# Kernel optimization log

Hardware: AMD Instinct MI355X
Metric: run time of the kernel (lower is better)

## Reference

```python
import jax, jax.numpy as jnp
import numpy as np

N_NODES = 200000
N_GRAPHS = 64
IRREPS = [(64, 1), (32, 3), (16, 5)]  # (mul, 2l+1); l==0 iff dim==1
EPS = 1e-05


def setup_inputs() -> dict:
    key = jax.random.key(0)
    k1, k2, k3, k4 = jax.random.split(key, 4)
    dim_total = sum(m * d for m, d in IRREPS)  # 240
    x = jax.random.normal(k1, (N_NODES, dim_total), dtype=jnp.float32)
    batch = jnp.sort(jax.random.randint(k2, (N_NODES,), 0, N_GRAPHS))
    weight = jax.random.uniform(k3, (sum(m for m, _ in IRREPS),), dtype=jnp.float32)  # [112]
    bias = jax.random.normal(k4, (sum(m for m, d in IRREPS if d == 1),), dtype=jnp.float32)  # [64]
    return {"x": x, "batch": batch, "weight": weight, "bias": bias}


def _segment_mean(v, batch, counts):
    s = jax.ops.segment_sum(v, batch, num_segments=N_GRAPHS)
    return s / counts.reshape((-1,) + (1,) * (v.ndim - 1))


def reference(x, batch, weight, bias):
    counts = jnp.maximum(
        jax.ops.segment_sum(jnp.ones_like(batch, dtype=x.dtype), batch, num_segments=N_GRAPHS), 1.0
    )  # [B]
    out = []
    ix = iw = ib = 0
    for mul, dim in IRREPS:
        field = x[:, ix : ix + mul * dim].reshape(-1, mul, dim)  # [N, mul, dim]
        # subtract_mean=True: per-graph mean over nodes, then over multiplicity
        mean = _segment_mean(field, batch, counts).mean(axis=1, keepdims=True)  # [B,1,dim]
        field = field - mean[batch]
        if dim == 1:  # divide_norm=False, but l==0 scalars always normalized
            norm = _segment_mean(field * field, batch, counts).mean(axis=(1, 2), keepdims=True)  # [B,1,1]
            field = field / (jnp.sqrt(norm)[batch] + EPS)
        field = field * weight[iw : iw + mul][None, :, None]
        if dim == 1:
            field = field + bias[ib : ib + mul][None, :, None]
            ib += mul
        out.append(field.reshape(-1, mul * dim))
        ix += mul * dim
        iw += mul
    return jnp.concatenate(out, axis=-1)
```

## Files before the change

### kernel.cpp

```cpp
#include <hip/hip_runtime.h>

#define NGRAPH 64
#define DIMT   240
#define DIMT4  60
#define EPS    1e-5f
#define ROWS   100

typedef float f32x4 __attribute__((ext_vector_type(4)));

__global__ __launch_bounds__(256) void stats_kernel(const float* __restrict__ x,
                                                    const int* __restrict__ batch,
                                                    float* __restrict__ gstats, int n)
{
    __shared__ int    sbatch[ROWS];
    __shared__ float4 ssum[240];
    __shared__ float4 ssq[64];
    __shared__ float  lstat[12];

    const int tid = threadIdx.x;
    const int r0 = blockIdx.x * ROWS;
    const int r1 = min(n, r0 + ROWS);
    if (r0 >= n) return;
    for (int i = tid; i < r1 - r0; i += 256) sbatch[i] = batch[r0 + i];
    __syncthreads();

    const bool active = tid < 240;
    const int  r_off  = tid / 60;
    const int  j      = tid - r_off * 60;
    const float4* x4  = (const float4*)x;

    int r = r0;
    while (r < r1) {
        const int b_cur = sbatch[r - r0];
        int lo = r + 1, hi = r1;
        while (lo < hi) {
            int mid = (lo + hi) >> 1;
            if (sbatch[mid - r0] <= b_cur) lo = mid + 1; else hi = mid;
        }
        const int r_end = lo;

        float4 sum = {0.f, 0.f, 0.f, 0.f};
        float4 sq  = {0.f, 0.f, 0.f, 0.f};
        if (active) {
            const bool dosq = (j < 16);
            int rbase = r;
            for (; rbase + 16 <= r_end; rbase += 16) {
                size_t i0 = (size_t)rbase * DIMT4 + tid;
                float4 v0 = x4[i0];
                float4 v1 = x4[i0 + 240];
                float4 v2 = x4[i0 + 480];
                float4 v3 = x4[i0 + 720];
                sum.x += (v0.x + v1.x) + (v2.x + v3.x);
                sum.y += (v0.y + v1.y) + (v2.y + v3.y);
                sum.z += (v0.z + v1.z) + (v2.z + v3.z);
                sum.w += (v0.w + v1.w) + (v2.w + v3.w);
                if (dosq) {
                    sq.x = fmaf(v0.x, v0.x, fmaf(v1.x, v1.x, fmaf(v2.x, v2.x, fmaf(v3.x, v3.x, sq.x))));
                    sq.y = fmaf(v0.y, v0.y, fmaf(v1.y, v1.y, fmaf(v2.y, v2.y, fmaf(v3.y, v3.y, sq.y))));
                    sq.z = fmaf(v0.z, v0.z, fmaf(v1.z, v1.z, fmaf(v2.z, v2.z, fmaf(v3.z, v3.z, sq.z))));
                    sq.w = fmaf(v0.w, v0.w, fmaf(v1.w, v1.w, fmaf(v2.w, v2.w, fmaf(v3.w, v3.w, sq.w))));
                }
            }
            for (; rbase < r_end; rbase += 4) {
                int rr = rbase + r_off;
                if (rr < r_end) {
                    float4 v = x4[(size_t)rr * DIMT4 + j];
                    sum.x += v.x; sum.y += v.y; sum.z += v.z; sum.w += v.w;
                    if (dosq) {
                        sq.x = fmaf(v.x, v.x, sq.x); sq.y = fmaf(v.y, v.y, sq.y);
                        sq.z = fmaf(v.z, v.z, sq.z); sq.w = fmaf(v.w, v.w, sq.w);
                    }
                }
            }
        }
        if (active) ssum[tid] = sum;
        if (active && j < 16) ssq[r_off * 16 + j] = sq;
        if (tid < 12) lstat[tid] = 0.f;
        __syncthreads();
        if (tid < 60) {
            float4 t0 = ssum[tid], t1 = ssum[60 + tid], t2 = ssum[120 + tid], t3 = ssum[180 + tid];
            float4 s4;
            s4.x = t0.x + t1.x + t2.x + t3.x;
            s4.y = t0.y + t1.y + t2.y + t3.y;
            s4.z = t0.z + t1.z + t2.z + t3.z;
            s4.w = t0.w + t1.w + t2.w + t3.w;
            if (tid < 16) {
                atomicAdd(&lstat[0], s4.x + s4.y + s4.z + s4.w);
                float4 q0 = ssq[tid], q1 = ssq[16 + tid], q2 = ssq[32 + tid], q3 = ssq[48 + tid];
                float qs = (q0.x + q0.y + q0.z + q0.w) + (q1.x + q1.y + q1.z + q1.w)
                         + (q2.x + q2.y + q2.z + q2.w) + (q3.x + q3.y + q3.z + q3.w);
                atomicAdd(&lstat[1], qs);
            } else if (tid < 40) {
                int base = 4 * tid - 64;
                atomicAdd(&lstat[2 + (base + 0) % 3], s4.x);
                atomicAdd(&lstat[2 + (base + 1) % 3], s4.y);
                atomicAdd(&lstat[2 + (base + 2) % 3], s4.z);
                atomicAdd(&lstat[2 + (base + 3) % 3], s4.w);
            } else {
                int base = 4 * tid - 160;
                atomicAdd(&lstat[5 + (base + 0) % 5], s4.x);
                atomicAdd(&lstat[5 + (base + 1) % 5], s4.y);
                atomicAdd(&lstat[5 + (base + 2) % 5], s4.z);
                atomicAdd(&lstat[5 + (base + 3) % 5], s4.w);
            }
        }
        __syncthreads();
        if (tid < 11) atomicAdd(gstats + b_cur * 12 + 1 + tid, lstat[tid]);
        if (tid == 0) atomicAdd(gstats + b_cur * 12 + 0, (float)(r_end - r));
        __syncthreads();
        r = r_end;
    }
}

__global__ __launch_bounds__(256) void finalize_kernel(const float* __restrict__ gstats,
                                                       const float* __restrict__ weight,
                                                       const float* __restrict__ bias,
                                                       float* __restrict__ A,
                                                       float* __restrict__ B)
{
    int b = blockIdx.x;
    int c = threadIdx.x;
    if (c >= DIMT) return;
    const float* st = gstats + b * 12;
    float cnt   = fmaxf(st[0], 1.f);
    float mean0 = st[1] / (cnt * 64.f);
    float ex2   = st[2] / (cnt * 64.f);
    float norm  = fmaxf(ex2 - mean0 * mean0, 0.f);
    float scale = 1.f / (sqrtf(norm) + EPS);
    float a, bb;
    if (c < 64) {
        float w = weight[c];
        a  = scale * w;
        bb = bias[c] - mean0 * a;
    } else if (c < 160) {
        int jj = c - 64;
        int d = jj % 3, m = jj / 3;
        float w = weight[64 + m];
        float mean = st[3 + d] / (cnt * 32.f);
        a = w; bb = -mean * w;
    } else {
        int jj = c - 160;
        int d = jj % 5, m = jj / 5;
        float w = weight[96 + m];
        float mean = st[6 + d] / (cnt * 16.f);
        a = w; bb = -mean * w;
    }
    A[b * DIMT + c] = a;
    B[b * DIMT + c] = bb;
}

__global__ __launch_bounds__(256) void apply_kernel(const float* __restrict__ x,
                                                    const int* __restrict__ batch,
                                                    const float* __restrict__ A,
                                                    const float* __restrict__ B,
                                                    float* __restrict__ out, int n)
{
    __shared__ int sbatch[ROWS];
    const int tid = threadIdx.x;
    const int r0 = blockIdx.x * ROWS;
    const int r1 = min(n, r0 + ROWS);
    if (r0 >= n) return;
    for (int i = tid; i < r1 - r0; i += 256) sbatch[i] = batch[r0 + i];
    __syncthreads();

    const bool active = tid < 240;
    const int  r_off  = tid / 60;
    const int  j      = tid - r_off * 60;
    const f32x4* x4   = (const f32x4*)x;
    f32x4*       o4   = (f32x4*)out;

    int r = r0;
    while (r < r1) {
        const int b_cur = sbatch[r - r0];
        int lo = r + 1, hi = r1;
        while (lo < hi) {
            int mid = (lo + hi) >> 1;
            if (sbatch[mid - r0] <= b_cur) lo = mid + 1; else hi = mid;
        }
        const int r_end = lo;

        if (active) {
            const f32x4 a  = ((const f32x4*)(A + b_cur * DIMT))[j];
            const f32x4 bb = ((const f32x4*)(B + b_cur * DIMT))[j];
            int rbase = r;
            for (; rbase + 16 <= r_end; rbase += 16) {
                size_t i0 = (size_t)rbase * DIMT4 + tid;
                f32x4 v0 = x4[i0];
                f32x4 v1 = x4[i0 + 240];
                f32x4 v2 = x4[i0 + 480];
                f32x4 v3 = x4[i0 + 720];
                f32x4 o0, o1, o2, o3;
                o0.x = fmaf(v0.x, a.x, bb.x); o0.y = fmaf(v0.y, a.y, bb.y);
                o0.z = fmaf(v0.z, a.z, bb.z); o0.w = fmaf(v0.w, a.w, bb.w);
                o1.x = fmaf(v1.x, a.x, bb.x); o1.y = fmaf(v1.y, a.y, bb.y);
                o1.z = fmaf(v1.z, a.z, bb.z); o1.w = fmaf(v1.w, a.w, bb.w);
                o2.x = fmaf(v2.x, a.x, bb.x); o2.y = fmaf(v2.y, a.y, bb.y);
                o2.z = fmaf(v2.z, a.z, bb.z); o2.w = fmaf(v2.w, a.w, bb.w);
                o3.x = fmaf(v3.x, a.x, bb.x); o3.y = fmaf(v3.y, a.y, bb.y);
                o3.z = fmaf(v3.z, a.z, bb.z); o3.w = fmaf(v3.w, a.w, bb.w);
                __builtin_nontemporal_store(o0, &o4[i0]);
                __builtin_nontemporal_store(o1, &o4[i0 + 240]);
                __builtin_nontemporal_store(o2, &o4[i0 + 480]);
                __builtin_nontemporal_store(o3, &o4[i0 + 720]);
            }
            for (; rbase < r_end; rbase += 4) {
                int rr = rbase + r_off;
                if (rr < r_end) {
                    size_t idx = (size_t)rr * DIMT4 + j;
                    f32x4 v = x4[idx];
                    f32x4 o;
                    o.x = fmaf(v.x, a.x, bb.x);
                    o.y = fmaf(v.y, a.y, bb.y);
                    o.z = fmaf(v.z, a.z, bb.z);
                    o.w = fmaf(v.w, a.w, bb.w);
                    __builtin_nontemporal_store(o, &o4[idx]);
                }
            }
        }
        r = r_end;
    }
}

extern "C" void kernel_launch(void* const* d_in, const int* in_sizes, int n_in,
                              void* d_out, int out_size, void* d_ws, size_t ws_size,
                              hipStream_t stream) {
    const float* x      = (const float*)d_in[0];
    const int*   batch  = (const int*)d_in[1];
    const float* weight = (const float*)d_in[2];
    const float* bias   = (const float*)d_in[3];
    float*       out    = (float*)d_out;
    int n = in_sizes[1];

    float* gstats = (float*)d_ws;
    float* A = (float*)((char*)d_ws + 4096);
    float* B = (float*)((char*)d_ws + 4096 + NGRAPH * DIMT * 4);

    hipMemsetAsync(d_ws, 0, NGRAPH * 12 * sizeof(float), stream);

    int nblocks = (n + ROWS - 1) / ROWS;
    stats_kernel<<<nblocks, 256, 0, stream>>>(x, batch, gstats, n);
    finalize_kernel<<<NGRAPH, 256, 0, stream>>>(gstats, weight, bias, A, B);
    apply_kernel<<<nblocks, 256, 0, stream>>>(x, batch, A, B, out, n);
}
```

Before: 362.3 us.

## Fuse stats, finalize and apply into one cooperative kernel with grid syncs

Replaces the memset plus three separate launches with a single cooperative kernel. Block 0 zeroes the per-graph statistics, and two grid-wide barriers separate the accumulation pass from the affine-apply pass. The per-column scale and shift are now computed inline from the statistics instead of through a separate finalize kernel and A/B buffers. Rows per block are doubled so the grid fits co-resident, and the old multi-kernel path is kept as a fallback if the cooperative launch fails. This trades launch and gap overhead for grid-sync cost, and it relies on every block being resident at once.

```diff
diff --git a/kernel.cpp b/kernel.cpp
--- a/kernel.cpp
+++ b/kernel.cpp
@@ -1,12 +1,229 @@
 #include <hip/hip_runtime.h>
+#include <hip/hip_cooperative_groups.h>
+
+namespace cg = cooperative_groups;
 
 #define NGRAPH 64
 #define DIMT   240
 #define DIMT4  60
 #define EPS    1e-5f
-#define ROWS   100
+#define ROWS   200
 
 typedef float f32x4 __attribute__((ext_vector_type(4)));
+
+struct AB { float a, b; };
+
+__device__ __forceinline__ AB affine_for_col(int c, const float* __restrict__ st,
+                                             float cnt,
+                                             const float* __restrict__ weight,
+                                             const float* __restrict__ bias)
+{
+    AB r;
+    if (c < 64) {
+        float mean0 = st[1] / (cnt * 64.f);
+        float ex2   = st[2] / (cnt * 64.f);
+        float norm  = fmaxf(ex2 - mean0 * mean0, 0.f);
+        float scale = 1.f / (sqrtf(norm) + EPS);
+        float w = weight[c];
+        r.a = scale * w;
+        r.b = bias[c] - mean0 * r.a;
+    } else if (c < 160) {
+        int jj = c - 64;
+        int d = jj % 3, m = jj / 3;
+        float w = weight[64 + m];
+        float mean = st[3 + d] / (cnt * 32.f);
+        r.a = w; r.b = -mean * w;
+    } else {
+        int jj = c - 160;
+        int d = jj % 5, m = jj / 5;
+        float w = weight[96 + m];
+        float mean = st[6 + d] / (cnt * 16.f);
+        r.a = w; r.b = -mean * w;
+    }
+    return r;
+}
+
+__global__ __launch_bounds__(256, 4) void fused_kernel(const float* __restrict__ x,
+                                                       const int* __restrict__ batch,
+                                                       const float* __restrict__ weight,
+                                                       const float* __restrict__ bias,
+                                                       float* __restrict__ out,
+                                                       float* __restrict__ gstats, int n)
+{
+    __shared__ int    sbatch[ROWS];
+    __shared__ float4 ssum[240];
+    __shared__ float4 ssq[64];
+    __shared__ float  lstat[12];
+
+    const int tid = threadIdx.x;
+    const int r0 = blockIdx.x * ROWS;
+    const int r1 = min(n, r0 + ROWS);
+    const bool has_work = (r0 < r1);
+
+    if (blockIdx.x == 0)
+        for (int i = tid; i < NGRAPH * 12; i += 256) gstats[i] = 0.f;
+
+    if (has_work) {
+        for (int i = tid; i < r1 - r0; i += 256) sbatch[i] = batch[r0 + i];
+        __syncthreads();
+    }
+
+    cg::this_grid().sync();
+
+    const bool active = tid < 240;
+    const int  r_off  = tid / 60;
+    const int  j      = tid - r_off * 60;
+    const f32x4* x4   = (const f32x4*)x;
+    f32x4*       o4   = (f32x4*)out;
+
+    if (has_work) {
+        int r = r0;
+        while (r < r1) {
+            const int b_cur = sbatch[r - r0];
+            int lo = r + 1, hi = r1;
+            while (lo < hi) {
+                int mid = (lo + hi) >> 1;
+                if (sbatch[mid - r0] <= b_cur) lo = mid + 1; else hi = mid;
+            }
+            const int r_end = lo;
+
+            f32x4 sum = {0.f, 0.f, 0.f, 0.f};
+            f32x4 sq  = {0.f, 0.f, 0.f, 0.f};
+            if (active) {
+                const bool dosq = (j < 16);
+                int rbase = r;
+                for (; rbase + 16 <= r_end; rbase += 16) {
+                    size_t i0 = (size_t)rbase * DIMT4 + tid;
+                    f32x4 v0 = x4[i0];
+                    f32x4 v1 = x4[i0 + 240];
+                    f32x4 v2 = x4[i0 + 480];
+                    f32x4 v3 = x4[i0 + 720];
+                    sum.x += (v0.x + v1.x) + (v2.x + v3.x);
+                    sum.y += (v0.y + v1.y) + (v2.y + v3.y);
+                    sum.z += (v0.z + v1.z) + (v2.z + v3.z);
+                    sum.w += (v0.w + v1.w) + (v2.w + v3.w);
+                    if (dosq) {
+                        sq.x = fmaf(v0.x, v0.x, fmaf(v1.x, v1.x, fmaf(v2.x, v2.x, fmaf(v3.x, v3.x, sq.x))));
+                        sq.y = fmaf(v0.y, v0.y, fmaf(v1.y, v1.y, fmaf(v2.y, v2.y, fmaf(v3.y, v3.y, sq.y))));
+                        sq.z = fmaf(v0.z, v0.z, fmaf(v1.z, v1.z, fmaf(v2.z, v2.z, fmaf(v3.z, v3.z, sq.z))));
+                        sq.w = fmaf(v0.w, v0.w, fmaf(v1.w, v1.w, fmaf(v2.w, v2.w, fmaf(v3.w, v3.w, sq.w))));
+                    }
+                }
+                for (; rbase < r_end; rbase += 4) {
+                    int rr = rbase + r_off;
+                    if (rr < r_end) {
+                        f32x4 v = x4[(size_t)rr * DIMT4 + j];
+                        sum.x += v.x; sum.y += v.y; sum.z += v.z; sum.w += v.w;
+                        if (dosq) {
+                            sq.x = fmaf(v.x, v.x, sq.x); sq.y = fmaf(v.y, v.y, sq.y);
+                            sq.z = fmaf(v.z, v.z, sq.z); sq.w = fmaf(v.w, v.w, sq.w);
+                        }
+                    }
+                }
+            }
+            if (active) { ssum[tid].x = sum.x; ssum[tid].y = sum.y; ssum[tid].z = sum.z; ssum[tid].w = sum.w; }
+            if (active && j < 16) { ssq[r_off * 16 + j].x = sq.x; ssq[r_off * 16 + j].y = sq.y;
+                                    ssq[r_off * 16 + j].z = sq.z; ssq[r_off * 16 + j].w = sq.w; }
+            if (tid < 12) lstat[tid] = 0.f;
+            __syncthreads();
+            if (tid < 60) {
+                float4 t0 = ssum[tid], t1 = ssum[60 + tid], t2 = ssum[120 + tid], t3 = ssum[180 + tid];
+                float4 s4;
+                s4.x = t0.x + t1.x + t2.x + t3.x;
+                s4.y = t0.y + t1.y + t2.y + t3.y;
+                s4.z = t0.z + t1.z + t2.z + t3.z;
+                s4.w = t0.w + t1.w + t2.w + t3.w;
+                if (tid < 16) {
+                    atomicAdd(&lstat[0], s4.x + s4.y + s4.z + s4.w);
+                    float4 q0 = ssq[tid], q1 = ssq[16 + tid], q2 = ssq[32 + tid], q3 = ssq[48 + tid];
+                    float qs = (q0.x + q0.y + q0.z + q0.w) + (q1.x + q1.y + q1.z + q1.w)
+                             + (q2.x + q2.y + q2.z + q2.w) + (q3.x + q3.y + q3.z + q3.w);
+                    atomicAdd(&lstat[1], qs);
+                } else if (tid < 40) {
+                    int base = 4 * tid - 64;
+                    atomicAdd(&lstat[2 + (base + 0) % 3], s4.x);
+                    atomicAdd(&lstat[2 + (base + 1) % 3], s4.y);
+                    atomicAdd(&lstat[2 + (base + 2) % 3], s4.z);
+                    atomicAdd(&lstat[2 + (base + 3) % 3], s4.w);
+                } else {
+                    int base = 4 * tid - 160;
+                    atomicAdd(&lstat[5 + (base + 0) % 5], s4.x);
+                    atomicAdd(&lstat[5 + (base + 1) % 5], s4.y);
+                    atomicAdd(&lstat[5 + (base + 2) % 5], s4.z);
+                    atomicAdd(&lstat[5 + (base + 3) % 5], s4.w);
+                }
+            }
+            __syncthreads();
+            if (tid < 11) atomicAdd(gstats + b_cur * 12 + 1 + tid, lstat[tid]);
+            if (tid == 0) atomicAdd(gstats + b_cur * 12 + 0, (float)(r_end - r));
+            __syncthreads();
+            r = r_end;
+        }
+    }
+
+    cg::this_grid().sync();
+
+    if (has_work) {
+        int r = r0;
+        while (r < r1) {
+            const int b_cur = sbatch[r - r0];
+            int lo = r + 1, hi = r1;
+            while (lo < hi) {
+                int mid = (lo + hi) >> 1;
+                if (sbatch[mid - r0] <= b_cur) lo = mid + 1; else hi = mid;
+            }
+            const int r_end = lo;
+
+            if (active) {
+                const float* st = gstats + b_cur * 12;
+                float cnt = fmaxf(st[0], 1.f);
+                AB c0 = affine_for_col(4 * j + 0, st, cnt, weight, bias);
+                AB c1 = affine_for_col(4 * j + 1, st, cnt, weight, bias);
+                AB c2 = affine_for_col(4 * j + 2, st, cnt, weight, bias);
+                AB c3 = affine_for_col(4 * j + 3, st, cnt, weight, bias);
+                f32x4 a, bb;
+                a.x = c0.a; a.y = c1.a; a.z = c2.a; a.w = c3.a;
+                bb.x = c0.b; bb.y = c1.b; bb.z = c2.b; bb.w = c3.b;
+
+                int rbase = r;
+                for (; rbase + 16 <= r_end; rbase += 16) {
+                    size_t i0 = (size_t)rbase * DIMT4 + tid;
+                    f32x4 v0 = x4[i0];
+                    f32x4 v1 = x4[i0 + 240];
+                    f32x4 v2 = x4[i0 + 480];
+                    f32x4 v3 = x4[i0 + 720];
+                    f32x4 o0, o1, o2, o3;
+                    o0.x = fmaf(v0.x, a.x, bb.x); o0.y = fmaf(v0.y, a.y, bb.y);
+                    o0.z = fmaf(v0.z, a.z, bb.z); o0.w = fmaf(v0.w, a.w, bb.w);
+                    o1.x = fmaf(v1.x, a.x, bb.x); o1.y = fmaf(v1.y, a.y, bb.y);
+                    o1.z = fmaf(v1.z, a.z, bb.z); o1.w = fmaf(v1.w, a.w, bb.w);
+                    o2.x = fmaf(v2.x, a.x, bb.x); o2.y = fmaf(v2.y, a.y, bb.y);
+                    o2.z = fmaf(v2.z, a.z, bb.z); o2.w = fmaf(v2.w, a.w, bb.w);
+                    o3.x = fmaf(v3.x, a.x, bb.x); o3.y = fmaf(v3.y, a.y, bb.y);
+                    o3.z = fmaf(v3.z, a.z, bb.z); o3.w = fmaf(v3.w, a.w, bb.w);
+                    __builtin_nontemporal_store(o0, &o4[i0]);
+                    __builtin_nontemporal_store(o1, &o4[i0 + 240]);
+                    __builtin_nontemporal_store(o2, &o4[i0 + 480]);
+                    __builtin_nontemporal_store(o3, &o4[i0 + 720]);
+                }
+                for (; rbase < r_end; rbase += 4) {
+                    int rr = rbase + r_off;
+                    if (rr < r_end) {
+                        size_t idx = (size_t)rr * DIMT4 + j;
+                        f32x4 v = x4[idx];
+                        f32x4 o;
+                        o.x = fmaf(v.x, a.x, bb.x);
+                        o.y = fmaf(v.y, a.y, bb.y);
+                        o.z = fmaf(v.z, a.z, bb.z);
+                        o.w = fmaf(v.w, a.w, bb.w);
+                        __builtin_nontemporal_store(o, &o4[idx]);
+                    }
+                }
+            }
+            r = r_end;
+        }
+    }
+}
 
 __global__ __launch_bounds__(256) void stats_kernel(const float* __restrict__ x,
                                                     const int* __restrict__ batch,
@@ -27,7 +244,7 @@
     const bool active = tid < 240;
     const int  r_off  = tid / 60;
     const int  j      = tid - r_off * 60;
-    const float4* x4  = (const float4*)x;
+    const f32x4* x4   = (const f32x4*)x;
 
     int r = r0;
     while (r < r1) {
@@ -39,17 +256,14 @@
         }
         const int r_end = lo;
 
-        float4 sum = {0.f, 0.f, 0.f, 0.f};
-        float4 sq  = {0.f, 0.f, 0.f, 0.f};
+        f32x4 sum = {0.f, 0.f, 0.f, 0.f};
+        f32x4 sq  = {0.f, 0.f, 0.f, 0.f};
         if (active) {
             const bool dosq = (j < 16);
             int rbase = r;
             for (; rbase + 16 <= r_end; rbase += 16) {
                 size_t i0 = (size_t)rbase * DIMT4 + tid;
-                float4 v0 = x4[i0];
-                float4 v1 = x4[i0 + 240];
-                float4 v2 = x4[i0 + 480];
-                float4 v3 = x4[i0 + 720];
+                f32x4 v0 = x4[i0], v1 = x4[i0 + 240], v2 = x4[i0 + 480], v3 = x4[i0 + 720];
                 sum.x += (v0.x + v1.x) + (v2.x + v3.x);
                 sum.y += (v0.y + v1.y) + (v2.y + v3.y);
                 sum.z += (v0.z + v1.z) + (v2.z + v3.z);
@@ -64,7 +278,7 @@
             for (; rbase < r_end; rbase += 4) {
                 int rr = rbase + r_off;
                 if (rr < r_end) {
-                    float4 v = x4[(size_t)rr * DIMT4 + j];
+                    f32x4 v = x4[(size_t)rr * DIMT4 + j];
                     sum.x += v.x; sum.y += v.y; sum.z += v.z; sum.w += v.w;
                     if (dosq) {
                         sq.x = fmaf(v.x, v.x, sq.x); sq.y = fmaf(v.y, v.y, sq.y);
@@ -73,8 +287,9 @@
                 }
             }
         }
-        if (active) ssum[tid] = sum;
-        if (active && j < 16) ssq[r_off * 16 + j] = sq;
+        if (active) { ssum[tid].x = sum.x; ssum[tid].y = sum.y; ssum[tid].z = sum.z; ssum[tid].w = sum.w; }
+        if (active && j < 16) { ssq[r_off * 16 + j].x = sq.x; ssq[r_off * 16 + j].y = sq.y;
+                                ssq[r_off * 16 + j].z = sq.z; ssq[r_off * 16 + j].w = sq.w; }
         if (tid < 12) lstat[tid] = 0.f;
         __syncthreads();
         if (tid < 60) {
@@ -112,47 +327,11 @@
     }
 }
 
-__global__ __launch_bounds__(256) void finalize_kernel(const float* __restrict__ gstats,
-                                                       const float* __restrict__ weight,
-                                                       const float* __restrict__ bias,
-                                                       float* __restrict__ A,
-                                                       float* __restrict__ B)
-{
-    int b = blockIdx.x;
-    int c = threadIdx.x;
-    if (c >= DIMT) return;
-    const float* st = gstats + b * 12;
-    float cnt   = fmaxf(st[0], 1.f);
-    float mean0 = st[1] / (cnt * 64.f);
-    float ex2   = st[2] / (cnt * 64.f);
-    float norm  = fmaxf(ex2 - mean0 * mean0, 0.f);
-    float scale = 1.f / (sqrtf(norm) + EPS);
-    float a, bb;
-    if (c < 64) {
-        float w = weight[c];
-        a  = scale * w;
-        bb = bias[c] - mean0 * a;
-    } else if (c < 160) {
-        int jj = c - 64;
-        int d = jj % 3, m = jj / 3;
-        float w = weight[64 + m];
-        float mean = st[3 + d] / (cnt * 32.f);
-        a = w; bb = -mean * w;
-    } else {
-        int jj = c - 160;
-        int d = jj % 5, m = jj / 5;
-        float w = weight[96 + m];
-        float mean = st[6 + d] / (cnt * 16.f);
-        a = w; bb = -mean * w;
-    }
-    A[b * DIMT + c] = a;
-    B[b * DIMT + c] = bb;
-}
-
 __global__ __launch_bounds__(256) void apply_kernel(const float* __restrict__ x,
                                                     const int* __restrict__ batch,
-                                                    const float* __restrict__ A,
-                                                    const float* __restrict__ B,
+                                                    const float* __restrict__ weight,
+                                                    const float* __restrict__ bias,
+                                                    const float* __restrict__ gstats,
                                                     float* __restrict__ out, int n)
 {
     __shared__ int sbatch[ROWS];
@@ -180,15 +359,20 @@
         const int r_end = lo;
 
         if (active) {
-            const f32x4 a  = ((const f32x4*)(A + b_cur * DIMT))[j];
-            const f32x4 bb = ((const f32x4*)(B + b_cur * DIMT))[j];
+            const float* st = gstats + b_cur * 12;
+            float cnt = fmaxf(st[0], 1.f);
+            AB c0 = affine_for_col(4 * j + 0, st, cnt, weight, bias);
+            AB c1 = affine_for_col(4 * j + 1, st, cnt, weight, bias);
+            AB c2 = affine_for_col(4 * j + 2, st, cnt, weight, bias);
+            AB c3 = affine_for_col(4 * j + 3, st, cnt, weight, bias);
+            f32x4 a, bb;
+            a.x = c0.a; a.y = c1.a; a.z = c2.a; a.w = c3.a;
+            bb.x = c0.b; bb.y = c1.b; bb.z = c2.b; bb.w = c3.b;
+
             int rbase = r;
             for (; rbase + 16 <= r_end; rbase += 16) {
                 size_t i0 = (size_t)rbase * DIMT4 + tid;
-                f32x4 v0 = x4[i0];
-                f32x4 v1 = x4[i0 + 240];
-                f32x4 v2 = x4[i0 + 480];
-                f32x4 v3 = x4[i0 + 720];
+                f32x4 v0 = x4[i0], v1 = x4[i0 + 240], v2 = x4[i0 + 480], v3 = x4[i0 + 720];
                 f32x4 o0, o1, o2, o3;
                 o0.x = fmaf(v0.x, a.x, bb.x); o0.y = fmaf(v0.y, a.y, bb.y);
                 o0.z = fmaf(v0.z, a.z, bb.z); o0.w = fmaf(v0.w, a.w, bb.w);
@@ -232,13 +416,17 @@
     int n = in_sizes[1];
 
     float* gstats = (float*)d_ws;
-    float* A = (float*)((char*)d_ws + 4096);
-    float* B = (float*)((char*)d_ws + 4096 + NGRAPH * DIMT * 4);
-
-    hipMemsetAsync(d_ws, 0, NGRAPH * 12 * sizeof(float), stream);
 
     int nblocks = (n + ROWS - 1) / ROWS;
-    stats_kernel<<<nblocks, 256, 0, stream>>>(x, batch, gstats, n);
-    finalize_kernel<<<NGRAPH, 256, 0, stream>>>(gstats, weight, bias, A, B);
-    apply_kernel<<<nblocks, 256, 0, stream>>>(x, batch, A, B, out, n);
+
+    void* params[7] = {(void*)&x, (void*)&batch, (void*)&weight, (void*)&bias,
+                       (void*)&out, (void*)&gstats, (void*)&n};
+    hipError_t err = hipLaunchCooperativeKernel((const void*)fused_kernel,
+                                                dim3(nblocks), dim3(256),
+                                                params, 0, stream);
+    if (err != hipSuccess) {
+        (void)hipMemsetAsync(gstats, 0, NGRAPH * 12 * sizeof(float), stream);
+        stats_kernel<<<nblocks, 256, 0, stream>>>(x, batch, gstats, n);
+        apply_kernel<<<nblocks, 256, 0, stream>>>(x, batch, weight, bias, gstats, out, n);
+    }
 }
```

Result: slower. 588.8 us (+62.5%).
